# Kernel optimization log

Measured on AMD Instinct MI355X. Metric: run time of the kernel, lower is better.

## Reference

```python
import jax, jax.numpy as jnp
import numpy as np

HS_ENC, HS_DEC, ATTN = 1024, 1024, 1024
N, T = 32, 2048


def setup_inputs() -> dict:
    key = jax.random.key(0)
    k1, k2, k3, k4, k5, k6 = jax.random.split(key, 6)
    h_dec = jax.random.normal(k1, (N, HS_DEC), dtype=jnp.float32)
    h_enc = jax.random.normal(k2, (N, T, HS_ENC), dtype=jnp.float32)
    src_lens = jax.random.randint(k3, (N,), 1, T + 1, dtype=jnp.int32)
    # params of nn.Linear(hs_enc+hs_dec, attn_size) and score vector v
    W = jax.random.normal(k4, (ATTN, HS_DEC + HS_ENC), dtype=jnp.float32) * 0.02
    b = jax.random.normal(k5, (ATTN,), dtype=jnp.float32) * 0.02
    v = jax.random.normal(k6, (ATTN,), dtype=jnp.float32)
    return {"h_dec": h_dec, "h_enc": h_enc, "src_lens": src_lens, "W": W, "b": b, "v": v}


def reference(h_dec, h_enc, src_lens, W, b, v):
    # Linear over concat(h_dec, h_enc) == sum of split projections; avoids
    # materializing the repeated/concatenated [N, T, hs_dec+hs_enc] tensor.
    hs_dec = h_dec.shape[-1]
    Wd, We = W[:, :hs_dec], W[:, hs_dec:]          # [A, hs_dec], [A, hs_enc]
    dec_proj = jnp.einsum('nd,ad->na', h_dec, Wd)  # [N, A]
    enc_proj = jnp.einsum('nte,ae->nta', h_enc, We)  # [N, T, A]
    attn_out = jnp.tanh(dec_proj[:, None, :] + enc_proj + b)  # [N, T, A]
    score = jnp.einsum('nta,a->nt', attn_out, v)   # [N, T]
    T_ = h_enc.shape[1]
    mask = jnp.arange(T_)[None, :] < src_lens[:, None]
    score = jnp.where(mask, score, jnp.float32(-1e10))
    weights = jax.nn.softmax(score, axis=-1)       # [N, T]
    ctx = jnp.einsum('nt,nte->ne', weights, h_enc) # [N, hs_enc]
    return ctx, weights
```

## Files before the change

### kernel.cpp

```cpp
#include <hip/hip_runtime.h>
#include <hip/hip_fp16.h>

#define HS 1024
#define TT 2048

typedef _Float16 half8 __attribute__((ext_vector_type(8)));
typedef float floatx4 __attribute__((ext_vector_type(4)));

__device__ __forceinline__ void dma16(const _Float16* g, _Float16* l) {
    __builtin_amdgcn_global_load_lds(
        (const __attribute__((address_space(1))) unsigned int*)g,
        (__attribute__((address_space(3))) unsigned int*)l, 16, 0, 0);
}

__global__ __launch_bounds__(256) void k_pre(const float* __restrict__ h_enc,
                                             _Float16* __restrict__ h_enc16,
                                             const float* __restrict__ h_dec,
                                             const float* __restrict__ W,
                                             const float* __restrict__ bias,
                                             const int* __restrict__ lens,
                                             float* __restrict__ dproj,
                                             _Float16* __restrict__ We16,
                                             float* __restrict__ sc,
                                             float* __restrict__ ctx) {
    const int b = blockIdx.x;
    const int tid = threadIdx.x;
    if (b < 16384) {
        const int n = b >> 9;
        const int t4 = (b & 511) * 4;
        const int lim = (lens[n] + 255) & ~255;
        if (t4 >= lim) return;
        size_t idx = ((size_t)b * 256 + tid) * 16;
        const float4* g = reinterpret_cast<const float4*>(h_enc + idx);
        _Float16 h[16];
#pragma unroll
        for (int i = 0; i < 4; ++i) {
            float4 f = g[i];
            h[i * 4 + 0] = (_Float16)f.x; h[i * 4 + 1] = (_Float16)f.y;
            h[i * 4 + 2] = (_Float16)f.z; h[i * 4 + 3] = (_Float16)f.w;
        }
        *reinterpret_cast<uint4*>(h_enc16 + idx)     = *reinterpret_cast<uint4*>(&h[0]);
        *reinterpret_cast<uint4*>(h_enc16 + idx + 8) = *reinterpret_cast<uint4*>(&h[8]);
    } else if (b < 24576) {
        int wid = (b - 16384) * 4 + (tid >> 6);
        int lane = tid & 63;
        int n = wid >> 10, a = wid & 1023;
        const float4* hd = reinterpret_cast<const float4*>(h_dec + (size_t)n * HS);
        const float4* wr = reinterpret_cast<const float4*>(W + (size_t)a * 2048);
        float s = 0.f;
#pragma unroll
        for (int i = 0; i < 4; ++i) {
            float4 h = hd[lane + i * 64];
            float4 w = wr[lane + i * 64];
            s += h.x * w.x + h.y * w.y + h.z * w.z + h.w * w.w;
        }
        for (int off = 32; off; off >>= 1) s += __shfl_xor(s, off);
        if (lane == 0) dproj[wid] = bias[a] + s;
    } else if (b < 25600) {
        int idx4 = ((b - 24576) * 256 + tid) * 4;
        int a = idx4 >> 10;
        int e = idx4 & 1023;
        float4 f = *reinterpret_cast<const float4*>(W + (size_t)a * 2048 + 1024 + e);
        _Float16 h0 = (_Float16)f.x, h1 = (_Float16)f.y, h2 = (_Float16)f.z, h3 = (_Float16)f.w;
        ushort4 p;
        p.x = *(unsigned short*)&h0; p.y = *(unsigned short*)&h1;
        p.z = *(unsigned short*)&h2; p.w = *(unsigned short*)&h3;
        *reinterpret_cast<ushort4*>(We16 + idx4) = p;
    } else if (b < 25664) {
        reinterpret_cast<float4*>(sc)[(b - 25600) * 256 + tid] =
            make_float4(0.f, 0.f, 0.f, 0.f);
    } else {
        reinterpret_cast<float4*>(ctx)[(b - 25664) * 256 + tid] =
            make_float4(0.f, 0.f, 0.f, 0.f);
    }
}

__global__ __launch_bounds__(512, 2) void k_score8(
        const _Float16* __restrict__ h_enc16, const _Float16* __restrict__ We16,
        const float* __restrict__ dproj, const float* __restrict__ v,
        const int* __restrict__ lens, float* __restrict__ scores) {
    __shared__ _Float16 As[4][256 * 32];
    __shared__ _Float16 Bs[4][256 * 32];
    __shared__ float s_acc[256];

    const int tid = threadIdx.x;
    const int ord = ((blockIdx.x & 7) << 7) | (blockIdx.x >> 3);
    const int aT = ord & 3, tT = (ord >> 2) & 7, n = ord >> 5;
    const int t0 = tT << 8, a0 = aT << 8;

    if (t0 >= lens[n]) return;

    if (tid < 256) s_acc[tid] = 0.0f;

    const int w = tid >> 6, lane = tid & 63;
    const int wm = w >> 2, wn = w & 3;
    const int col = lane & 15, quad = lane >> 4;

    const _Float16* srcA[2];
    const _Float16* srcB[2];
#pragma unroll
    for (int c = 0; c < 2; ++c) {
        int Gp = c * 512 + tid;
        int Gl = Gp ^ ((Gp >> 3) & 7);
        int r = Gl >> 2, g = Gl & 3;
        srcA[c] = h_enc16 + ((size_t)(n * TT + t0 + r)) * HS + g * 8;
        srcB[c] = We16 + ((size_t)(a0 + r)) * HS + g * 8;
    }

    int offA[8], offB[4];
#pragma unroll
    for (int mi = 0; mi < 8; ++mi) {
        int r = wm * 128 + mi * 16 + col;
        offA[mi] = (r * 64 + quad * 16) ^ (((r >> 1) & 7) << 4);
    }
#pragma unroll
    for (int ni = 0; ni < 4; ++ni) {
        int r = wn * 64 + ni * 16 + col;
        offB[ni] = (r * 64 + quad * 16) ^ (((r >> 1) & 7) << 4);
    }

    floatx4 acc[8][4];
#pragma unroll
    for (int mi = 0; mi < 8; ++mi)
#pragma unroll
        for (int ni = 0; ni < 4; ++ni) acc[mi][ni] = (floatx4)0.0f;

    auto issue2 = [&](int kt, int c) {
        const int b = kt & 3;
        dma16(srcA[c] + kt * 32, &As[b][c * 4096 + w * 512]);
        dma16(srcB[c] + kt * 32, &Bs[b][c * 4096 + w * 512]);
    };

#pragma unroll
    for (int kt = 0; kt < 3; ++kt) { issue2(kt, 0); issue2(kt, 1); }

    for (int kt = 0; kt < 32; ++kt) {
        const int b = kt & 3;
        if (kt < 30)       asm volatile("s_waitcnt vmcnt(8)" ::: "memory");
        else if (kt == 30) asm volatile("s_waitcnt vmcnt(4)" ::: "memory");
        else               asm volatile("s_waitcnt vmcnt(0)" ::: "memory");
        __builtin_amdgcn_s_barrier();
        __builtin_amdgcn_sched_barrier(0);

        const char* Ab = (const char*)As[b];
        const char* Bb = (const char*)Bs[b];
        half8 af[4], bf[4];
#pragma unroll
        for (int ni = 0; ni < 4; ++ni)
            bf[ni] = *reinterpret_cast<const half8*>(Bb + offB[ni]);
#pragma unroll
        for (int mi = 0; mi < 4; ++mi)
            af[mi] = *reinterpret_cast<const half8*>(Ab + offA[mi]);
        if (kt < 29) issue2(kt + 3, 0);
        __builtin_amdgcn_s_setprio(1);
#pragma unroll
        for (int mi = 0; mi < 4; ++mi)
#pragma unroll
            for (int ni = 0; ni < 4; ++ni)
                acc[mi][ni] = __builtin_amdgcn_mfma_f32_16x16x32_f16(
                    af[mi], bf[ni], acc[mi][ni], 0, 0, 0);
        __builtin_amdgcn_s_setprio(0);

#pragma unroll
        for (int mi = 0; mi < 4; ++mi)
            af[mi] = *reinterpret_cast<const half8*>(Ab + offA[4 + mi]);
        if (kt < 29) issue2(kt + 3, 1);
        __builtin_amdgcn_s_setprio(1);
#pragma unroll
        for (int mi = 0; mi < 4; ++mi)
#pragma unroll
            for (int ni = 0; ni < 4; ++ni)
                acc[4 + mi][ni] = __builtin_amdgcn_mfma_f32_16x16x32_f16(
                    af[mi], bf[ni], acc[4 + mi][ni], 0, 0, 0);
        __builtin_amdgcn_s_setprio(0);
    }

    float vv[4], dd[4];
#pragma unroll
    for (int ni = 0; ni < 4; ++ni) {
        const int a = a0 + wn * 64 + ni * 16 + col;
        vv[ni] = v[a];
        dd[ni] = dproj[n * HS + a];
    }
#pragma unroll
    for (int mi = 0; mi < 8; ++mi) {
#pragma unroll
        for (int rg = 0; rg < 4; ++rg) {
            float s = 0.0f;
#pragma unroll
            for (int ni = 0; ni < 4; ++ni) {
                float x = acc[mi][ni][rg] + dd[ni];
                float e2 = __expf(2.0f * x);
                float th = 1.0f - 2.0f * __builtin_amdgcn_rcpf(e2 + 1.0f);
                s += vv[ni] * th;
            }
            s += __shfl_xor(s, 8);
            s += __shfl_xor(s, 4);
            s += __shfl_xor(s, 2);
            s += __shfl_xor(s, 1);
            if (col == 0)
                atomicAdd(&s_acc[wm * 128 + mi * 16 + quad * 4 + rg], s);
        }
    }
    __syncthreads();
    if (tid < 256)
        atomicAdd(&scores[(size_t)n * TT + t0 + tid], s_acc[tid]);
}

__global__ __launch_bounds__(256) void k_ctxsm(const _Float16* __restrict__ h_enc16,
                                               const float* __restrict__ sc,
                                               const int* __restrict__ lens,
                                               float* __restrict__ wts,
                                               float* __restrict__ ctx) {
    __shared__ float red[4], red2[4];
    __shared__ float racc[256][8];
    const int b = blockIdx.x;
    const int n = b >> 4, ec = (b >> 2) & 3, ts = b & 3;
    const int tid = threadIdx.x;
    const int len = lens[n];
    const float* srow = sc + (size_t)n * TT;

    float sv[8];
    float m = -3.0e38f;
#pragma unroll
    for (int i = 0; i < 8; ++i) {
        int t = tid + i * 256;
        float s = srow[t];
        s = (t < len) ? s : -1.0e10f;
        sv[i] = s;
        m = fmaxf(m, s);
    }
    for (int off = 1; off <= 32; off <<= 1) m = fmaxf(m, __shfl_xor(m, off));
    if ((tid & 63) == 0) red[tid >> 6] = m;
    __syncthreads();
    m = fmaxf(fmaxf(red[0], red[1]), fmaxf(red[2], red[3]));
    float sum = 0.f;
#pragma unroll
    for (int i = 0; i < 8; ++i) sum += __expf(sv[i] - m);
    for (int off = 1; off <= 32; off <<= 1) sum += __shfl_xor(sum, off);
    if ((tid & 63) == 0) red2[tid >> 6] = sum;
    __syncthreads();
    sum = red2[0] + red2[1] + red2[2] + red2[3];
    const float rinv = 1.0f / sum;

    if (ec == 0) {
#pragma unroll
        for (int j = 0; j < 2; ++j) {
            int t = ts * 512 + j * 256 + tid;
            float s = srow[t];
            s = (t < len) ? s : -1.0e10f;
            wts[(size_t)n * TT + t] = __expf(s - m) * rinv;
        }
    }

    if (ts * 512 < len) {
        const int tend = min(ts * 512 + 512, len);
        const int q = tid & 31, tg = tid >> 5;
        const int e = ec * 256 + q * 8;
        float acc[8];
#pragma unroll
        for (int j = 0; j < 8; ++j) acc[j] = 0.f;
        for (int t = ts * 512 + tg; t < tend; t += 8) {
            float w = __expf(srow[t] - m) * rinv;
            uint4 raw = *reinterpret_cast<const uint4*>(
                h_enc16 + ((size_t)(n * TT + t)) * HS + e);
            const _Float16* hp = reinterpret_cast<const _Float16*>(&raw);
#pragma unroll
            for (int j = 0; j < 8; ++j) acc[j] += w * (float)hp[j];
        }
#pragma unroll
        for (int j = 0; j < 8; ++j) racc[tid][j] = acc[j];
        __syncthreads();
        if (tid < 32) {
            float s2[8];
#pragma unroll
            for (int j = 0; j < 8; ++j) s2[j] = racc[tid][j];
            for (int g = 1; g < 8; ++g)
#pragma unroll
                for (int j = 0; j < 8; ++j) s2[j] += racc[g * 32 + tid][j];
            float* dst = ctx + (size_t)n * HS + ec * 256 + tid * 8;
#pragma unroll
            for (int j = 0; j < 8; ++j) atomicAdd(dst + j, s2[j]);
        }
    }
}

__global__ __launch_bounds__(256) void k_dproj(const float* __restrict__ h_dec,
                                               const float* __restrict__ W,
                                               const float* __restrict__ bias,
                                               float* __restrict__ dproj) {
    int wid = blockIdx.x * 4 + (threadIdx.x >> 6);
    int lane = threadIdx.x & 63;
    int n = wid >> 10, a = wid & 1023;
    const float4* hd = reinterpret_cast<const float4*>(h_dec + (size_t)n * HS);
    const float4* wr = reinterpret_cast<const float4*>(W + (size_t)a * 2048);
    float s = 0.f;
#pragma unroll
    for (int i = 0; i < 4; ++i) {
        float4 h = hd[lane + i * 64];
        float4 w = wr[lane + i * 64];
        s += h.x * w.x + h.y * w.y + h.z * w.z + h.w * w.w;
    }
    for (int off = 32; off; off >>= 1) s += __shfl_xor(s, off);
    if (lane == 0) dproj[wid] = bias[a] + s;
}

__global__ __launch_bounds__(256) void k_cvtW(const float* __restrict__ W,
                                              _Float16* __restrict__ We16) {
    int idx4 = (blockIdx.x * 256 + threadIdx.x) * 4;
    int a = idx4 >> 10;
    int e = idx4 & 1023;
    float4 f = *reinterpret_cast<const float4*>(W + (size_t)a * 2048 + 1024 + e);
    _Float16 h0 = (_Float16)f.x, h1 = (_Float16)f.y, h2 = (_Float16)f.z, h3 = (_Float16)f.w;
    ushort4 p;
    p.x = *(unsigned short*)&h0; p.y = *(unsigned short*)&h1;
    p.z = *(unsigned short*)&h2; p.w = *(unsigned short*)&h3;
    *reinterpret_cast<ushort4*>(We16 + idx4) = p;
}

__global__ __launch_bounds__(256) void k_cvtA(const float* __restrict__ h_enc,
                                              _Float16* __restrict__ h_enc16) {
    size_t idx = ((size_t)blockIdx.x * 256 + threadIdx.x) * 16;
    const float4* g = reinterpret_cast<const float4*>(h_enc + idx);
    _Float16 h[16];
#pragma unroll
    for (int i = 0; i < 4; ++i) {
        float4 f = g[i];
        h[i * 4 + 0] = (_Float16)f.x; h[i * 4 + 1] = (_Float16)f.y;
        h[i * 4 + 2] = (_Float16)f.z; h[i * 4 + 3] = (_Float16)f.w;
    }
    *reinterpret_cast<uint4*>(h_enc16 + idx)     = *reinterpret_cast<uint4*>(&h[0]);
    *reinterpret_cast<uint4*>(h_enc16 + idx + 8) = *reinterpret_cast<uint4*>(&h[8]);
}

__global__ __launch_bounds__(256) void k_softmax(float* __restrict__ wout,
                                                 const int* __restrict__ lens) {
    __shared__ float red[4];
    __shared__ float red2[4];
    int n = blockIdx.x, tid = threadIdx.x;
    int len = lens[n];
    float* row = wout + (size_t)n * TT;
    float sv[8];
    float m = -3.0e38f;
#pragma unroll
    for (int i = 0; i < 8; ++i) {
        int t = tid + i * 256;
        float s = row[t];
        s = (t < len) ? s : -1.0e10f;
        sv[i] = s;
        m = fmaxf(m, s);
    }
    for (int off = 1; off <= 32; off <<= 1) m = fmaxf(m, __shfl_xor(m, off));
    if ((tid & 63) == 0) red[tid >> 6] = m;
    __syncthreads();
    m = fmaxf(fmaxf(red[0], red[1]), fmaxf(red[2], red[3]));
    float sum = 0.f, es[8];
#pragma unroll
    for (int i = 0; i < 8; ++i) { es[i] = __expf(sv[i] - m); sum += es[i]; }
    for (int off = 1; off <= 32; off <<= 1) sum += __shfl_xor(sum, off);
    if ((tid & 63) == 0) red2[tid >> 6] = sum;
    __syncthreads();
    sum = red2[0] + red2[1] + red2[2] + red2[3];
    float rinv = 1.0f / sum;
#pragma unroll
    for (int i = 0; i < 8; ++i) row[tid + i * 256] = es[i] * rinv;
}

__global__ __launch_bounds__(256) void k_ctx(const _Float16* __restrict__ h_enc16,
                                             const float* __restrict__ wts,
                                             float* __restrict__ ctx) {
    __shared__ float red[256][8];
    int b = blockIdx.x;
    int n  = b >> 4;
    int ec = (b >> 2) & 3;
    int ts = b & 3;
    int tid = threadIdx.x;
    int q = tid & 31, tg = tid >> 5;
    int e = ec * 256 + q * 8;
    float acc[8];
#pragma unroll
    for (int j = 0; j < 8; ++j) acc[j] = 0.f;
    const float* wrow = wts + (size_t)n * TT;
    for (int t = ts * 512 + tg; t < ts * 512 + 512; t += 8) {
        float w = wrow[t];
        uint4 raw = *reinterpret_cast<const uint4*>(
            h_enc16 + ((size_t)(n * TT + t)) * HS + e);
        const _Float16* hp = reinterpret_cast<const _Float16*>(&raw);
#pragma unroll
        for (int j = 0; j < 8; ++j) acc[j] += w * (float)hp[j];
    }
#pragma unroll
    for (int j = 0; j < 8; ++j) red[tid][j] = acc[j];
    __syncthreads();
    if (tid < 32) {
        float s[8];
#pragma unroll
        for (int j = 0; j < 8; ++j) s[j] = red[tid][j];
        for (int g = 1; g < 8; ++g)
#pragma unroll
            for (int j = 0; j < 8; ++j) s[j] += red[g * 32 + tid][j];
        float* dst = ctx + (size_t)n * HS + ec * 256 + tid * 8;
#pragma unroll
        for (int j = 0; j < 8; ++j) atomicAdd(dst + j, s[j]);
    }
}

__global__ __launch_bounds__(256) void k_score_naive(const float* __restrict__ h_enc,
                                                     const float* __restrict__ W,
                                                     const float* __restrict__ dproj,
                                                     const float* __restrict__ v,
                                                     float* __restrict__ scores) {
    int gw = blockIdx.x * 4 + (threadIdx.x >> 6);
    int lane = threadIdx.x & 63;
    int n = gw >> 11, t = gw & 2047;
    const float4* he = reinterpret_cast<const float4*>(h_enc + ((size_t)(n * TT + t)) * HS);
    float4 hv[4];
#pragma unroll
    for (int i = 0; i < 4; ++i) hv[i] = he[lane + i * 64];
    float s = 0.f;
    for (int a = 0; a < 1024; ++a) {
        const float4* wr = reinterpret_cast<const float4*>(W + (size_t)a * 2048 + 1024);
        float d = 0.f;
#pragma unroll
        for (int i = 0; i < 4; ++i) {
            float4 wv = wr[lane + i * 64];
            d += hv[i].x * wv.x + hv[i].y * wv.y + hv[i].z * wv.z + hv[i].w * wv.w;
        }
        for (int off = 32; off; off >>= 1) d += __shfl_xor(d, off);
        s += v[a] * tanhf(d + dproj[n * HS + a]);
    }
    if (lane == 0) scores[(size_t)n * TT + t] = s;
}

__global__ __launch_bounds__(256) void k_ctx_naive(const float* __restrict__ h_enc,
                                                   const float* __restrict__ wts,
                                                   float* __restrict__ ctx) {
    int n = blockIdx.x;
    int e = threadIdx.x * 4;
    float4 a = make_float4(0.f, 0.f, 0.f, 0.f);
    const float* wrow = wts + (size_t)n * TT;
    for (int t = 0; t < TT; ++t) {
        float w = wrow[t];
        float4 h = *reinterpret_cast<const float4*>(h_enc + ((size_t)(n * TT + t)) * HS + e);
        a.x += w * h.x; a.y += w * h.y; a.z += w * h.z; a.w += w * h.w;
    }
    *reinterpret_cast<float4*>(ctx + (size_t)n * HS + e) = a;
}

extern "C" void kernel_launch(void* const* d_in, const int* in_sizes, int n_in,
                              void* d_out, int out_size, void* d_ws, size_t ws_size,
                              hipStream_t stream) {
    const float* h_dec    = (const float*)d_in[0];
    const float* h_enc    = (const float*)d_in[1];
    const int*   src_lens = (const int*)d_in[2];
    const float* W = (const float*)d_in[3];
    const float* b = (const float*)d_in[4];
    const float* v = (const float*)d_in[5];

    float* out = (float*)d_out;
    float* ctx = out;
    float* wts = out + 32 * 1024;

    float*    dproj   = (float*)d_ws;
    _Float16* We16    = (_Float16*)((char*)d_ws + 131072);
    _Float16* h_enc16 = (_Float16*)((char*)d_ws + 131072 + 2097152);
    float*    sc      = (float*)((char*)d_ws + 131072 + 2097152 +
                                 (size_t)32 * TT * HS * 2);
    const size_t need_mid = 131072 + 2097152 + (size_t)32 * TT * HS * 2;
    const size_t need_new = need_mid + (size_t)32 * TT * sizeof(float);

    if (ws_size >= need_new) {
        k_pre   <<<25696, 256, 0, stream>>>(h_enc, h_enc16, h_dec, W, b, src_lens,
                                            dproj, We16, sc, ctx);
        k_score8<<<1024, 512, 0, stream>>>(h_enc16, We16, dproj, v, src_lens, sc);
        k_ctxsm <<<512, 256, 0, stream>>>(h_enc16, sc, src_lens, wts, ctx);
    } else if (ws_size >= need_mid) {
        k_dproj<<<8192, 256, 0, stream>>>(h_dec, W, b, dproj);
        (void)hipMemsetAsync(ctx, 0, 32 * 1024 * sizeof(float), stream);
        (void)hipMemsetAsync(wts, 0, (size_t)32 * TT * sizeof(float), stream);
        k_cvtW <<<1024, 256, 0, stream>>>(W, We16);
        k_cvtA <<<16384, 256, 0, stream>>>(h_enc, h_enc16);
        k_score8<<<1024, 512, 0, stream>>>(h_enc16, We16, dproj, v, src_lens, wts);
        k_softmax<<<32, 256, 0, stream>>>(wts, src_lens);
        k_ctx  <<<512, 256, 0, stream>>>(h_enc16, wts, ctx);
    } else {
        k_dproj<<<8192, 256, 0, stream>>>(h_dec, W, b, dproj);
        k_score_naive<<<16384, 256, 0, stream>>>(h_enc, W, dproj, v, wts);
        k_softmax<<<32, 256, 0, stream>>>(wts, src_lens);
        k_ctx_naive<<<32, 256, 0, stream>>>(h_enc, wts, ctx);
    }
}
```

Baseline: 492.5 us.

## Pack valid timesteps across batches into dense 128-row tiles for score GEMM

Builds a compaction table in the preprocessing kernel that maps packed row indices to (batch, t) for all valid timesteps, so the score GEMM processes only the sum of lengths rounded to 128 rather than per-batch padding to 256. The GEMM tile shrinks to 128x128 with 256 threads and a 3-stage buffer, and rows are gathered through the table, with dproj looked up per row in the epilogue. The h_enc conversion is trimmed to exact lengths, and the mid-workspace fallback path is removed. This cuts wasted MFMA work on masked rows but adds indirect gathers, per-row dproj loads, and a serial 32-batch loop per table entry.

```diff
diff --git a/kernel.cpp b/kernel.cpp
--- a/kernel.cpp
+++ b/kernel.cpp
@@ -22,14 +22,14 @@
                                              float* __restrict__ dproj,
                                              _Float16* __restrict__ We16,
                                              float* __restrict__ sc,
-                                             float* __restrict__ ctx) {
+                                             float* __restrict__ ctx,
+                                             int* __restrict__ tbl) {
     const int b = blockIdx.x;
     const int tid = threadIdx.x;
     if (b < 16384) {
         const int n = b >> 9;
         const int t4 = (b & 511) * 4;
-        const int lim = (lens[n] + 255) & ~255;
-        if (t4 >= lim) return;
+        if (t4 >= lens[n]) return;
         size_t idx = ((size_t)b * 256 + tid) * 16;
         const float4* g = reinterpret_cast<const float4*>(h_enc + idx);
         _Float16 h[16];
@@ -69,48 +69,72 @@
     } else if (b < 25664) {
         reinterpret_cast<float4*>(sc)[(b - 25600) * 256 + tid] =
             make_float4(0.f, 0.f, 0.f, 0.f);
-    } else {
+    } else if (b < 25696) {
         reinterpret_cast<float4*>(ctx)[(b - 25664) * 256 + tid] =
             make_float4(0.f, 0.f, 0.f, 0.f);
-    }
-}
-
-__global__ __launch_bounds__(512, 2) void k_score8(
+    } else {
+        const int bi = b - 25696;
+        const int v0 = bi * 1024 + tid * 4;
+        int vals[4] = {-1, -1, -1, -1};
+        int base = 0;
+        for (int n = 0; n < 32; ++n) {
+            const int ln = lens[n];
+#pragma unroll
+            for (int k2 = 0; k2 < 4; ++k2) {
+                const int vv = v0 + k2;
+                if (vv >= base && vv < base + ln) vals[k2] = n * TT + (vv - base);
+            }
+            base += ln;
+        }
+        *reinterpret_cast<int4*>(tbl + v0) = make_int4(vals[0], vals[1], vals[2], vals[3]);
+    }
+}
+
+__global__ __launch_bounds__(256, 3) void k_score8(
         const _Float16* __restrict__ h_enc16, const _Float16* __restrict__ We16,
         const float* __restrict__ dproj, const float* __restrict__ v,
-        const int* __restrict__ lens, float* __restrict__ scores) {
-    __shared__ _Float16 As[4][256 * 32];
-    __shared__ _Float16 Bs[4][256 * 32];
-    __shared__ float s_acc[256];
+        const int* __restrict__ lens, const int* __restrict__ tbl,
+        float* __restrict__ scores) {
+    __shared__ _Float16 As[3][128 * 32];
+    __shared__ _Float16 Bs[3][128 * 32];
+    __shared__ float s_acc[128];
 
     const int tid = threadIdx.x;
-    const int ord = ((blockIdx.x & 7) << 7) | (blockIdx.x >> 3);
-    const int aT = ord & 3, tT = (ord >> 2) & 7, n = ord >> 5;
-    const int t0 = tT << 8, a0 = aT << 8;
-
-    if (t0 >= lens[n]) return;
-
-    if (tid < 256) s_acc[tid] = 0.0f;
-
-    const int w = tid >> 6, lane = tid & 63;
-    const int wm = w >> 2, wn = w & 3;
+    const int lane = tid & 63;
+
+    int S = (lane < 32) ? lens[lane] : 0;
+#pragma unroll
+    for (int off = 1; off <= 32; off <<= 1) S += __shfl_xor(S, off);
+    const int Tt = (S + 127) >> 7;
+
+    const int ord = ((blockIdx.x & 7) << 9) | (blockIdx.x >> 3);
+    const int aT = ord & 7, tile = ord >> 3;
+    if (tile >= Tt) return;
+    const int t0 = tile << 7, a0 = aT << 7;
+
+    if (tid < 128) s_acc[tid] = 0.0f;
+
+    const int w = tid >> 6;
+    const int wm = w >> 1, wn = w & 1;
     const int col = lane & 15, quad = lane >> 4;
 
     const _Float16* srcA[2];
     const _Float16* srcB[2];
 #pragma unroll
     for (int c = 0; c < 2; ++c) {
-        int Gp = c * 512 + tid;
+        int Gp = c * 256 + tid;
         int Gl = Gp ^ ((Gp >> 3) & 7);
         int r = Gl >> 2, g = Gl & 3;
-        srcA[c] = h_enc16 + ((size_t)(n * TT + t0 + r)) * HS + g * 8;
+        int grow = tbl[t0 + r];
+        if (grow < 0) grow = 0;
+        srcA[c] = h_enc16 + (size_t)grow * HS + g * 8;
         srcB[c] = We16 + ((size_t)(a0 + r)) * HS + g * 8;
     }
 
-    int offA[8], offB[4];
-#pragma unroll
-    for (int mi = 0; mi < 8; ++mi) {
-        int r = wm * 128 + mi * 16 + col;
+    int offA[4], offB[4];
+#pragma unroll
+    for (int mi = 0; mi < 4; ++mi) {
+        int r = wm * 64 + mi * 16 + col;
         offA[mi] = (r * 64 + quad * 16) ^ (((r >> 1) & 7) << 4);
     }
 #pragma unroll
@@ -119,39 +143,40 @@
         offB[ni] = (r * 64 + quad * 16) ^ (((r >> 1) & 7) << 4);
     }
 
-    floatx4 acc[8][4];
-#pragma unroll
-    for (int mi = 0; mi < 8; ++mi)
+    floatx4 acc[4][4];
+#pragma unroll
+    for (int mi = 0; mi < 4; ++mi)
 #pragma unroll
         for (int ni = 0; ni < 4; ++ni) acc[mi][ni] = (floatx4)0.0f;
 
-    auto issue2 = [&](int kt, int c) {
-        const int b = kt & 3;
-        dma16(srcA[c] + kt * 32, &As[b][c * 4096 + w * 512]);
-        dma16(srcB[c] + kt * 32, &Bs[b][c * 4096 + w * 512]);
+    auto issue = [&](int kt) {
+        const int bb = kt % 3;
+#pragma unroll
+        for (int c = 0; c < 2; ++c) {
+            dma16(srcA[c] + kt * 32, &As[bb][(c * 256 + w * 64) * 8]);
+            dma16(srcB[c] + kt * 32, &Bs[bb][(c * 256 + w * 64) * 8]);
+        }
     };
 
-#pragma unroll
-    for (int kt = 0; kt < 3; ++kt) { issue2(kt, 0); issue2(kt, 1); }
-
-    for (int kt = 0; kt < 32; ++kt) {
-        const int b = kt & 3;
-        if (kt < 30)       asm volatile("s_waitcnt vmcnt(8)" ::: "memory");
-        else if (kt == 30) asm volatile("s_waitcnt vmcnt(4)" ::: "memory");
-        else               asm volatile("s_waitcnt vmcnt(0)" ::: "memory");
+    issue(0);
+    issue(1);
+
+    for (int j = 0; j < 31; ++j) {
+        asm volatile("s_waitcnt vmcnt(4)" ::: "memory");
         __builtin_amdgcn_s_barrier();
         __builtin_amdgcn_sched_barrier(0);
 
-        const char* Ab = (const char*)As[b];
-        const char* Bb = (const char*)Bs[b];
+        const int bb = j % 3;
+        const char* Ab = (const char*)As[bb];
+        const char* Bb = (const char*)Bs[bb];
         half8 af[4], bf[4];
+#pragma unroll
+        for (int mi = 0; mi < 4; ++mi)
+            af[mi] = *reinterpret_cast<const half8*>(Ab + offA[mi]);
 #pragma unroll
         for (int ni = 0; ni < 4; ++ni)
             bf[ni] = *reinterpret_cast<const half8*>(Bb + offB[ni]);
-#pragma unroll
-        for (int mi = 0; mi < 4; ++mi)
-            af[mi] = *reinterpret_cast<const half8*>(Ab + offA[mi]);
-        if (kt < 29) issue2(kt + 3, 0);
+        if (j < 30) issue(j + 2);
         __builtin_amdgcn_s_setprio(1);
 #pragma unroll
         for (int mi = 0; mi < 4; ++mi)
@@ -160,36 +185,45 @@
                 acc[mi][ni] = __builtin_amdgcn_mfma_f32_16x16x32_f16(
                     af[mi], bf[ni], acc[mi][ni], 0, 0, 0);
         __builtin_amdgcn_s_setprio(0);
-
+    }
+    {
+        asm volatile("s_waitcnt vmcnt(0)" ::: "memory");
+        __builtin_amdgcn_s_barrier();
+        __builtin_amdgcn_sched_barrier(0);
+        const char* Ab = (const char*)As[31 % 3];
+        const char* Bb = (const char*)Bs[31 % 3];
+        half8 af[4], bf[4];
 #pragma unroll
         for (int mi = 0; mi < 4; ++mi)
-            af[mi] = *reinterpret_cast<const half8*>(Ab + offA[4 + mi]);
-        if (kt < 29) issue2(kt + 3, 1);
+            af[mi] = *reinterpret_cast<const half8*>(Ab + offA[mi]);
+#pragma unroll
+        for (int ni = 0; ni < 4; ++ni)
+            bf[ni] = *reinterpret_cast<const half8*>(Bb + offB[ni]);
         __builtin_amdgcn_s_setprio(1);
 #pragma unroll
         for (int mi = 0; mi < 4; ++mi)
 #pragma unroll
             for (int ni = 0; ni < 4; ++ni)
-                acc[4 + mi][ni] = __builtin_amdgcn_mfma_f32_16x16x32_f16(
-                    af[mi], bf[ni], acc[4 + mi][ni], 0, 0, 0);
+                acc[mi][ni] = __builtin_amdgcn_mfma_f32_16x16x32_f16(
+                    af[mi], bf[ni], acc[mi][ni], 0, 0, 0);
         __builtin_amdgcn_s_setprio(0);
     }
 
-    float vv[4], dd[4];
-#pragma unroll
-    for (int ni = 0; ni < 4; ++ni) {
-        const int a = a0 + wn * 64 + ni * 16 + col;
-        vv[ni] = v[a];
-        dd[ni] = dproj[n * HS + a];
-    }
-#pragma unroll
-    for (int mi = 0; mi < 8; ++mi) {
+    float vv[4];
+#pragma unroll
+    for (int ni = 0; ni < 4; ++ni) vv[ni] = v[a0 + wn * 64 + ni * 16 + col];
+#pragma unroll
+    for (int mi = 0; mi < 4; ++mi) {
 #pragma unroll
         for (int rg = 0; rg < 4; ++rg) {
+            const int rloc = wm * 64 + mi * 16 + quad * 4 + rg;
+            const int rv = tbl[t0 + rloc];
+            const int n0 = (rv < 0) ? 0 : (rv >> 11);
+            const float* dp = dproj + (size_t)n0 * HS + a0 + wn * 64 + col;
             float s = 0.0f;
 #pragma unroll
             for (int ni = 0; ni < 4; ++ni) {
-                float x = acc[mi][ni][rg] + dd[ni];
+                float x = acc[mi][ni][rg] + dp[ni * 16];
                 float e2 = __expf(2.0f * x);
                 float th = 1.0f - 2.0f * __builtin_amdgcn_rcpf(e2 + 1.0f);
                 s += vv[ni] * th;
@@ -198,13 +232,14 @@
             s += __shfl_xor(s, 4);
             s += __shfl_xor(s, 2);
             s += __shfl_xor(s, 1);
-            if (col == 0)
-                atomicAdd(&s_acc[wm * 128 + mi * 16 + quad * 4 + rg], s);
+            if (col == 0) atomicAdd(&s_acc[rloc], s);
         }
     }
     __syncthreads();
-    if (tid < 256)
-        atomicAdd(&scores[(size_t)n * TT + t0 + tid], s_acc[tid]);
+    if (tid < 128) {
+        const int rv = tbl[t0 + tid];
+        if (rv >= 0) atomicAdd(&scores[rv], s_acc[tid]);
+    }
 }
 
 __global__ __launch_bounds__(256) void k_ctxsm(const _Float16* __restrict__ h_enc16,
@@ -305,106 +340,6 @@
     if (lane == 0) dproj[wid] = bias[a] + s;
 }
 
-__global__ __launch_bounds__(256) void k_cvtW(const float* __restrict__ W,
-                                              _Float16* __restrict__ We16) {
-    int idx4 = (blockIdx.x * 256 + threadIdx.x) * 4;
-    int a = idx4 >> 10;
-    int e = idx4 & 1023;
-    float4 f = *reinterpret_cast<const float4*>(W + (size_t)a * 2048 + 1024 + e);
-    _Float16 h0 = (_Float16)f.x, h1 = (_Float16)f.y, h2 = (_Float16)f.z, h3 = (_Float16)f.w;
-    ushort4 p;
-    p.x = *(unsigned short*)&h0; p.y = *(unsigned short*)&h1;
-    p.z = *(unsigned short*)&h2; p.w = *(unsigned short*)&h3;
-    *reinterpret_cast<ushort4*>(We16 + idx4) = p;
-}
-
-__global__ __launch_bounds__(256) void k_cvtA(const float* __restrict__ h_enc,
-                                              _Float16* __restrict__ h_enc16) {
-    size_t idx = ((size_t)blockIdx.x * 256 + threadIdx.x) * 16;
-    const float4* g = reinterpret_cast<const float4*>(h_enc + idx);
-    _Float16 h[16];
-#pragma unroll
-    for (int i = 0; i < 4; ++i) {
-        float4 f = g[i];
-        h[i * 4 + 0] = (_Float16)f.x; h[i * 4 + 1] = (_Float16)f.y;
-        h[i * 4 + 2] = (_Float16)f.z; h[i * 4 + 3] = (_Float16)f.w;
-    }
-    *reinterpret_cast<uint4*>(h_enc16 + idx)     = *reinterpret_cast<uint4*>(&h[0]);
-    *reinterpret_cast<uint4*>(h_enc16 + idx + 8) = *reinterpret_cast<uint4*>(&h[8]);
-}
-
-__global__ __launch_bounds__(256) void k_softmax(float* __restrict__ wout,
-                                                 const int* __restrict__ lens) {
-    __shared__ float red[4];
-    __shared__ float red2[4];
-    int n = blockIdx.x, tid = threadIdx.x;
-    int len = lens[n];
-    float* row = wout + (size_t)n * TT;
-    float sv[8];
-    float m = -3.0e38f;
-#pragma unroll
-    for (int i = 0; i < 8; ++i) {
-        int t = tid + i * 256;
-        float s = row[t];
-        s = (t < len) ? s : -1.0e10f;
-        sv[i] = s;
-        m = fmaxf(m, s);
-    }
-    for (int off = 1; off <= 32; off <<= 1) m = fmaxf(m, __shfl_xor(m, off));
-    if ((tid & 63) == 0) red[tid >> 6] = m;
-    __syncthreads();
-    m = fmaxf(fmaxf(red[0], red[1]), fmaxf(red[2], red[3]));
-    float sum = 0.f, es[8];
-#pragma unroll
-    for (int i = 0; i < 8; ++i) { es[i] = __expf(sv[i] - m); sum += es[i]; }
-    for (int off = 1; off <= 32; off <<= 1) sum += __shfl_xor(sum, off);
-    if ((tid & 63) == 0) red2[tid >> 6] = sum;
-    __syncthreads();
-    sum = red2[0] + red2[1] + red2[2] + red2[3];
-    float rinv = 1.0f / sum;
-#pragma unroll
-    for (int i = 0; i < 8; ++i) row[tid + i * 256] = es[i] * rinv;
-}
-
-__global__ __launch_bounds__(256) void k_ctx(const _Float16* __restrict__ h_enc16,
-                                             const float* __restrict__ wts,
-                                             float* __restrict__ ctx) {
-    __shared__ float red[256][8];
-    int b = blockIdx.x;
-    int n  = b >> 4;
-    int ec = (b >> 2) & 3;
-    int ts = b & 3;
-    int tid = threadIdx.x;
-    int q = tid & 31, tg = tid >> 5;
-    int e = ec * 256 + q * 8;
-    float acc[8];
-#pragma unroll
-    for (int j = 0; j < 8; ++j) acc[j] = 0.f;
-    const float* wrow = wts + (size_t)n * TT;
-    for (int t = ts * 512 + tg; t < ts * 512 + 512; t += 8) {
-        float w = wrow[t];
-        uint4 raw = *reinterpret_cast<const uint4*>(
-            h_enc16 + ((size_t)(n * TT + t)) * HS + e);
-        const _Float16* hp = reinterpret_cast<const _Float16*>(&raw);
-#pragma unroll
-        for (int j = 0; j < 8; ++j) acc[j] += w * (float)hp[j];
-    }
-#pragma unroll
-    for (int j = 0; j < 8; ++j) red[tid][j] = acc[j];
-    __syncthreads();
-    if (tid < 32) {
-        float s[8];
-#pragma unroll
-        for (int j = 0; j < 8; ++j) s[j] = red[tid][j];
-        for (int g = 1; g < 8; ++g)
-#pragma unroll
-            for (int j = 0; j < 8; ++j) s[j] += red[g * 32 + tid][j];
-        float* dst = ctx + (size_t)n * HS + ec * 256 + tid * 8;
-#pragma unroll
-        for (int j = 0; j < 8; ++j) atomicAdd(dst + j, s[j]);
-    }
-}
-
 __global__ __launch_bounds__(256) void k_score_naive(const float* __restrict__ h_enc,
                                                      const float* __restrict__ W,
                                                      const float* __restrict__ dproj,
@@ -430,6 +365,39 @@
         s += v[a] * tanhf(d + dproj[n * HS + a]);
     }
     if (lane == 0) scores[(size_t)n * TT + t] = s;
+}
+
+__global__ __launch_bounds__(256) void k_softmax(float* __restrict__ wout,
+                                                 const int* __restrict__ lens) {
+    __shared__ float red[4];
+    __shared__ float red2[4];
+    int n = blockIdx.x, tid = threadIdx.x;
+    int len = lens[n];
+    float* row = wout + (size_t)n * TT;
+    float sv[8];
+    float m = -3.0e38f;
+#pragma unroll
+    for (int i = 0; i < 8; ++i) {
+        int t = tid + i * 256;
+        float s = row[t];
+        s = (t < len) ? s : -1.0e10f;
+        sv[i] = s;
+        m = fmaxf(m, s);
+    }
+    for (int off = 1; off <= 32; off <<= 1) m = fmaxf(m, __shfl_xor(m, off));
+    if ((tid & 63) == 0) red[tid >> 6] = m;
+    __syncthreads();
+    m = fmaxf(fmaxf(red[0], red[1]), fmaxf(red[2], red[3]));
+    float sum = 0.f, es[8];
+#pragma unroll
+    for (int i = 0; i < 8; ++i) { es[i] = __expf(sv[i] - m); sum += es[i]; }
+    for (int off = 1; off <= 32; off <<= 1) sum += __shfl_xor(sum, off);
+    if ((tid & 63) == 0) red2[tid >> 6] = sum;
+    __syncthreads();
+    sum = red2[0] + red2[1] + red2[2] + red2[3];
+    float rinv = 1.0f / sum;
+#pragma unroll
+    for (int i = 0; i < 8; ++i) row[tid + i * 256] = es[i] * rinv;
 }
 
 __global__ __launch_bounds__(256) void k_ctx_naive(const float* __restrict__ h_enc,
@@ -463,26 +431,16 @@
 
     float*    dproj   = (float*)d_ws;
     _Float16* We16    = (_Float16*)((char*)d_ws + 131072);
-    _Float16* h_enc16 = (_Float16*)((char*)d_ws + 131072 + 2097152);
-    float*    sc      = (float*)((char*)d_ws + 131072 + 2097152 +
-                                 (size_t)32 * TT * HS * 2);
-    const size_t need_mid = 131072 + 2097152 + (size_t)32 * TT * HS * 2;
-    const size_t need_new = need_mid + (size_t)32 * TT * sizeof(float);
+    _Float16* h_enc16 = (_Float16*)((char*)d_ws + 2228224);
+    float*    sc      = (float*)((char*)d_ws + 136445952);
+    int*      tbl     = (int*)((char*)d_ws + 136708096);
+    const size_t need_new = 136970240;
 
     if (ws_size >= need_new) {
-        k_pre   <<<25696, 256, 0, stream>>>(h_enc, h_enc16, h_dec, W, b, src_lens,
-                                            dproj, We16, sc, ctx);
-        k_score8<<<1024, 512, 0, stream>>>(h_enc16, We16, dproj, v, src_lens, sc);
+        k_pre   <<<25760, 256, 0, stream>>>(h_enc, h_enc16, h_dec, W, b, src_lens,
+                                            dproj, We16, sc, ctx, tbl);
+        k_score8<<<4096, 256, 0, stream>>>(h_enc16, We16, dproj, v, src_lens, tbl, sc);
         k_ctxsm <<<512, 256, 0, stream>>>(h_enc16, sc, src_lens, wts, ctx);
-    } else if (ws_size >= need_mid) {
-        k_dproj<<<8192, 256, 0, stream>>>(h_dec, W, b, dproj);
-        (void)hipMemsetAsync(ctx, 0, 32 * 1024 * sizeof(float), stream);
-        (void)hipMemsetAsync(wts, 0, (size_t)32 * TT * sizeof(float), stream);
-        k_cvtW <<<1024, 256, 0, stream>>>(W, We16);
-        k_cvtA <<<16384, 256, 0, stream>>>(h_enc, h_enc16);
-        k_score8<<<1024, 512, 0, stream>>>(h_enc16, We16, dproj, v, src_lens, wts);
-        k_softmax<<<32, 256, 0, stream>>>(wts, src_lens);
-        k_ctx  <<<512, 256, 0, stream>>>(h_enc16, wts, ctx);
     } else {
         k_dproj<<<8192, 256, 0, stream>>>(h_dec, W, b, dproj);
         k_score_naive<<<16384, 256, 0, stream>>>(h_enc, W, dproj, v, wts);
```

After: 552.3 us. 12.1% more time.
